# Performance work log

Hardware: AMD Instinct MI355X
Metric: run time of the kernel (lower is better)

Reference implementation:

```python
import jax, jax.numpy as jnp
import numpy as np

B, C, N = 8, 512, 2048  # batch, channels (=size), tokens


def setup_inputs() -> dict:
    key = jax.random.key(0)
    ks = jax.random.split(key, 9)
    s = 1.0 / np.sqrt(C)
    return {
        "q": jax.random.normal(ks[0], (B, C, N), dtype=jnp.float32),
        "k": jax.random.normal(ks[1], (B, C, N), dtype=jnp.float32),
        "v": jax.random.normal(ks[2], (B, C, N), dtype=jnp.float32),
        "wq": jax.random.normal(ks[3], (C, C), dtype=jnp.float32) * s,
        "bq": jax.random.normal(ks[4], (C,), dtype=jnp.float32) * s,
        "wk": jax.random.normal(ks[5], (C, C), dtype=jnp.float32) * s,
        "bk": jax.random.normal(ks[6], (C,), dtype=jnp.float32) * s,
        "wv": jax.random.normal(ks[7], (C, C), dtype=jnp.float32) * s,
        "bv": jax.random.normal(ks[8], (C,), dtype=jnp.float32) * s,
    }


def _proj(x, w, b):
    # 1x1 conv over channels: out[b,c,n] = sum_i w[c,i] x[b,i,n] + b[c]
    return jnp.einsum('ci,bin->bcn', w, x) + b[None, :, None]


def reference(q, k, v, wq, bq, wk, bk, wv, bv):
    residual = q                                   # [B, C, N]
    qp = _proj(q, wq, bq).transpose(0, 2, 1)       # [B, N, C]
    kp = _proj(k, wk, bk).transpose(0, 2, 1)       # [B, N, C]
    vp = _proj(v, wv, bv).transpose(0, 2, 1)       # [B, N, C]
    attn = jnp.einsum('bnc,bmc->bnm', qp, kp)      # raw QK^T, no scale/softmax
    out = jnp.einsum('bnm,bmc->bnc', attn, vp)     # [B, N, C]
    return out.transpose(0, 2, 1) + residual       # [B, C, N]
```

## Files before the change

kernel.cpp:

```cpp
#include <hip/hip_runtime.h>
#include <hip/hip_bf16.h>
#include <stdint.h>

#define B_ 8
#define C_ 512
#define N_ 2048

typedef __bf16 bf16_t;
typedef bf16_t bf16x8 __attribute__((ext_vector_type(8)));
typedef bf16_t bf16x4 __attribute__((ext_vector_type(4)));
typedef float f32x4 __attribute__((ext_vector_type(4)));

__global__ __launch_bounds__(256) void prep_qw_kernel(
    const float* __restrict__ q,
    const float* __restrict__ wq, const float* __restrict__ wk,
    const float* __restrict__ wv, const float* __restrict__ bq,
    const float* __restrict__ bk,
    bf16_t* __restrict__ qT,
    bf16_t* __restrict__ WqT, bf16_t* __restrict__ WkT, bf16_t* __restrict__ Wvb,
    float* __restrict__ s1p)
{
    __shared__ bf16_t tile[64][65];
    __shared__ float red256[256];
    const int bid = blockIdx.x;
    const int tid = threadIdx.x;

    if (bid < 2048) {
        const int b = bid >> 8;
        const int rem = bid & 255;
        const int c0 = (rem >> 5) * 64;
        const int n0 = (rem & 31) * 64;
        const float* src = q + (size_t)b * C_ * N_;
        bf16_t* dT = qT + (size_t)b * N_ * C_;
        const int cx = (tid & 15) * 4, ry = tid >> 4;
#pragma unroll
        for (int r = ry; r < 64; r += 16) {
            float4 f = *(const float4*)&src[(size_t)(c0 + r) * N_ + n0 + cx];
            tile[r][cx + 0] = (bf16_t)f.x; tile[r][cx + 1] = (bf16_t)f.y;
            tile[r][cx + 2] = (bf16_t)f.z; tile[r][cx + 3] = (bf16_t)f.w;
        }
        __syncthreads();
#pragma unroll
        for (int r = ry; r < 64; r += 16) {
            bf16x4 o;
            o[0] = tile[cx + 0][r]; o[1] = tile[cx + 1][r];
            o[2] = tile[cx + 2][r]; o[3] = tile[cx + 3][r];
            *(bf16x4*)&dT[(size_t)(n0 + r) * C_ + c0 + cx] = o;
        }
    } else if (bid < 2176) {
        const int t = bid - 2048;
        const float* src = (t < 64) ? wq : wk;
        bf16_t* dst = (t < 64) ? WqT : WkT;
        const int j = t & 63;
        const int i0 = (j & 7) * 64, c0 = (j >> 3) * 64;
        const int cx = (tid & 15) * 4, ry = tid >> 4;
#pragma unroll
        for (int r = ry; r < 64; r += 16) {
            float4 f = *(const float4*)&src[(size_t)(c0 + r) * C_ + i0 + cx];
            tile[r][cx + 0] = (bf16_t)f.x; tile[r][cx + 1] = (bf16_t)f.y;
            tile[r][cx + 2] = (bf16_t)f.z; tile[r][cx + 3] = (bf16_t)f.w;
        }
        __syncthreads();
#pragma unroll
        for (int r = ry; r < 64; r += 16) {
            bf16x4 o;
            o[0] = tile[cx + 0][r]; o[1] = tile[cx + 1][r];
            o[2] = tile[cx + 2][r]; o[3] = tile[cx + 3][r];
            *(bf16x4*)&dst[(size_t)(i0 + r) * C_ + c0 + cx] = o;
        }
    } else if (bid < 2240) {
        const int j = bid - 2176;
#pragma unroll
        for (int p = 0; p < 4; ++p) {
            const int i = j * 4096 + p * 1024 + tid * 4;
            float4 f = *(const float4*)(wv + i);
            bf16x4 o;
            o[0] = (bf16_t)f.x; o[1] = (bf16_t)f.y;
            o[2] = (bf16_t)f.z; o[3] = (bf16_t)f.w;
            *(bf16x4*)(Wvb + i) = o;
        }
    } else {
        float p = bk[tid] * bq[tid] + bk[tid + 256] * bq[tid + 256];
        red256[tid] = p;
        __syncthreads();
        for (int s = 128; s > 0; s >>= 1) {
            if (tid < s) red256[tid] += red256[tid + s];
            __syncthreads();
        }
        if (tid == 0) s1p[0] = red256[0];
    }
}

__global__ __launch_bounds__(256) void dkv_M_kernel(
    const float* __restrict__ Kin, const float* __restrict__ Vin,
    bf16_t* __restrict__ Dp, float* __restrict__ sk4, float* __restrict__ sv4,
    const bf16_t* __restrict__ WqT, const bf16_t* __restrict__ WkT,
    bf16_t* __restrict__ M, const float* __restrict__ bq,
    const float* __restrict__ bk, float* __restrict__ gk,
    float* __restrict__ va)
{
    __shared__ __align__(16) float AsF[128 * 64];
    __shared__ __align__(16) float BsF[128 * 64];

    const int f = blockIdx.x;
    const int tid = threadIdx.x, lane = tid & 63, wave = tid >> 6;
    const int wr = wave >> 1, wc = wave & 1;
    const size_t sCC = (size_t)C_ * C_;

    if (f < 512) {
        const int xcd = f & 7, sl = f >> 3;
        const int g = xcd + 8 * (sl >> 4), t5 = sl & 15;
        const int bz = g >> 2, sp = g & 3;
        const int m0 = (t5 >> 2) * 128, n0 = (t5 & 3) * 128;
        const int kbeg = sp * 512;

        const float* Ab = Kin + (size_t)bz * C_ * N_;
        const float* Bb = Vin + (size_t)bz * C_ * N_;

        f32x4 acc[4][4];
#pragma unroll
        for (int i = 0; i < 4; ++i)
#pragma unroll
            for (int j = 0; j < 4; ++j) acc[i][j] = 0.f;

        const int prow = tid >> 4;
        const int cs   = (tid & 15) ^ (prow & 7);
        const int ldso = tid * 16;

        const int srr = tid >> 1, hh = tid & 1;
        float hsA = 0.f, hsB = 0.f;
        const bool doA = (n0 == 0), doB = (m0 == 0);

        for (int t = 0; t < 8; ++t) {
            const float* ga = Ab + (size_t)(m0 + prow) * N_ + kbeg + t * 64 + cs * 4;
            const float* gb = Bb + (size_t)(n0 + prow) * N_ + kbeg + t * 64 + cs * 4;
#pragma unroll
            for (int p = 0; p < 8; ++p)
                __builtin_amdgcn_global_load_lds(
                    (const __attribute__((address_space(1))) void*)(ga + (size_t)p * 16 * N_),
                    (__attribute__((address_space(3))) void*)((char*)AsF + ldso + p * 4096),
                    16, 0, 0);
#pragma unroll
            for (int p = 0; p < 8; ++p)
                __builtin_amdgcn_global_load_lds(
                    (const __attribute__((address_space(1))) void*)(gb + (size_t)p * 16 * N_),
                    (__attribute__((address_space(3))) void*)((char*)BsF + ldso + p * 4096),
                    16, 0, 0);
            __syncthreads();

#pragma unroll
            for (int kk = 0; kk < 64; kk += 32) {
                bf16x8 af[4], bfr[4];
                const int kcol = kk + (lane >> 4) * 8;
                const int c1 = kcol >> 2;
#pragma unroll
                for (int m = 0; m < 4; ++m) {
                    const int r = wr * 64 + (lane & 15) + m * 16;
                    f32x4 lo = *(const f32x4*)((const char*)AsF + r * 256 + ((c1 ^ (r & 7)) << 4));
                    f32x4 hi = *(const f32x4*)((const char*)AsF + r * 256 + (((c1 + 1) ^ (r & 7)) << 4));
                    bf16x8 fr;
                    fr[0] = (bf16_t)lo[0]; fr[1] = (bf16_t)lo[1];
                    fr[2] = (bf16_t)lo[2]; fr[3] = (bf16_t)lo[3];
                    fr[4] = (bf16_t)hi[0]; fr[5] = (bf16_t)hi[1];
                    fr[6] = (bf16_t)hi[2]; fr[7] = (bf16_t)hi[3];
                    af[m] = fr;
                }
#pragma unroll
                for (int n = 0; n < 4; ++n) {
                    const int r = wc * 64 + (lane & 15) + n * 16;
                    f32x4 lo = *(const f32x4*)((const char*)BsF + r * 256 + ((c1 ^ (r & 7)) << 4));
                    f32x4 hi = *(const f32x4*)((const char*)BsF + r * 256 + (((c1 + 1) ^ (r & 7)) << 4));
                    bf16x8 fr;
                    fr[0] = (bf16_t)lo[0]; fr[1] = (bf16_t)lo[1];
                    fr[2] = (bf16_t)lo[2]; fr[3] = (bf16_t)lo[3];
                    fr[4] = (bf16_t)hi[0]; fr[5] = (bf16_t)hi[1];
                    fr[6] = (bf16_t)hi[2]; fr[7] = (bf16_t)hi[3];
                    bfr[n] = fr;
                }
#pragma unroll
                for (int m = 0; m < 4; ++m)
#pragma unroll
                    for (int n = 0; n < 4; ++n)
                        acc[m][n] = __builtin_amdgcn_mfma_f32_16x16x32_bf16(
                            af[m], bfr[n], acc[m][n], 0, 0, 0);
            }

            if (doA) {
#pragma unroll
                for (int u = 0; u < 8; ++u) {
                    const int slot = ((hh * 8 + u) + srr) & 15;
                    f32x4 vv = *(const f32x4*)((const char*)AsF + srr * 256 + slot * 16);
                    hsA += vv[0] + vv[1] + vv[2] + vv[3];
                }
            }
            if (doB) {
#pragma unroll
                for (int u = 0; u < 8; ++u) {
                    const int slot = ((hh * 8 + u) + srr) & 15;
                    f32x4 vv = *(const f32x4*)((const char*)BsF + srr * 256 + slot * 16);
                    hsB += vv[0] + vv[1] + vv[2] + vv[3];
                }
            }
            __syncthreads();
        }

        const int rj = (lane >> 4) * 4;
        const int cc = lane & 15;
        const int z = bz * 4 + sp;
#pragma unroll
        for (int m = 0; m < 4; ++m)
#pragma unroll
            for (int n = 0; n < 4; ++n) {
                const int col = n0 + wc * 64 + n * 16 + cc;
                f32x4 vv = acc[m][n];
#pragma unroll
                for (int j = 0; j < 4; ++j) {
                    const int row = m0 + wr * 64 + m * 16 + rj + j;
                    Dp[(size_t)z * sCC + (size_t)row * C_ + col] = (bf16_t)vv[j];
                }
            }
        if (doA) {
            hsA += __shfl_xor(hsA, 1, 64);
            if (!hh) sk4[(size_t)(sp * B_ + bz) * C_ + m0 + srr] = hsA;
        }
        if (doB) {
            hsB += __shfl_xor(hsB, 1, 64);
            if (!hh) sv4[(size_t)(sp * B_ + bz) * C_ + n0 + srr] = hsB;
        }
    } else if (f < 576) {
        bf16_t* As = (bf16_t*)AsF;
        bf16_t* Bs = (bf16_t*)BsF;
        const int g = f - 512;
        const int m0 = (g >> 3) * 64, n0 = (g & 7) * 64;
        f32x4 acc[2][2];
#pragma unroll
        for (int i = 0; i < 2; ++i)
#pragma unroll
            for (int j = 0; j < 2; ++j) acc[i][j] = 0.f;
        const int srow = tid >> 3;
        const int scol = ((tid & 7) ^ (srow & 7)) * 8;
        const int ldso = tid * 16;
        for (int t = 0; t < 8; ++t) {
            const bf16_t* ga = WqT + (size_t)(m0 + srow) * C_ + t * 64 + scol;
            const bf16_t* gb = WkT + (size_t)(n0 + srow) * C_ + t * 64 + scol;
#pragma unroll
            for (int p = 0; p < 2; ++p)
                __builtin_amdgcn_global_load_lds(
                    (const __attribute__((address_space(1))) void*)(ga + (size_t)p * 32 * C_),
                    (__attribute__((address_space(3))) void*)((char*)As + ldso + p * 4096),
                    16, 0, 0);
#pragma unroll
            for (int p = 0; p < 2; ++p)
                __builtin_amdgcn_global_load_lds(
                    (const __attribute__((address_space(1))) void*)(gb + (size_t)p * 32 * C_),
                    (__attribute__((address_space(3))) void*)((char*)Bs + ldso + p * 4096),
                    16, 0, 0);
            __syncthreads();
#pragma unroll
            for (int kk = 0; kk < 64; kk += 32) {
                bf16x8 af[2], bfr[2];
                const int kcol = kk + (lane >> 4) * 8;
                const int kcn = kcol >> 3;
#pragma unroll
                for (int m = 0; m < 2; ++m) {
                    const int r = wr * 32 + (lane & 15) + m * 16;
                    af[m] = *(const bf16x8*)((const char*)As + r * 128 +
                                             ((kcn ^ (r & 7)) << 4));
                }
#pragma unroll
                for (int n = 0; n < 2; ++n) {
                    const int r = wc * 32 + (lane & 15) + n * 16;
                    bfr[n] = *(const bf16x8*)((const char*)Bs + r * 128 +
                                              ((kcn ^ (r & 7)) << 4));
                }
#pragma unroll
                for (int m = 0; m < 2; ++m)
#pragma unroll
                    for (int n = 0; n < 2; ++n)
                        acc[m][n] = __builtin_amdgcn_mfma_f32_16x16x32_bf16(
                            af[m], bfr[n], acc[m][n], 0, 0, 0);
            }
            __syncthreads();
        }
        const int rj = (lane >> 4) * 4;
        const int cc = lane & 15;
#pragma unroll
        for (int m = 0; m < 2; ++m)
#pragma unroll
            for (int n = 0; n < 2; ++n) {
                const int col = n0 + wc * 32 + n * 16 + cc;
                f32x4 vv = acc[m][n];
#pragma unroll
                for (int j = 0; j < 4; ++j) {
                    const int row = m0 + wr * 32 + m * 16 + rj + j;
                    M[(size_t)row * C_ + col] = (bf16_t)vv[j];
                }
            }
    } else {
        const int j = f - 576;
        const bf16_t* W = (j < 8) ? WkT : WqT;
        const float* bb = (j < 8) ? bq : bk;
        float* out = (j < 8) ? gk : va;
        const int row = (j & 7) * 64 + (tid >> 2);
        const int c0 = (tid & 3) * 128;
        const bf16_t* rp = W + (size_t)row * C_ + c0;
        float acc = 0.f;
#pragma unroll
        for (int e = 0; e < 128; e += 8) {
            bf16x8 vv = *(const bf16x8*)(rp + e);
#pragma unroll
            for (int x = 0; x < 8; ++x) acc += (float)vv[x] * bb[c0 + e + x];
        }
        acc += __shfl_xor(acc, 1, 64);
        acc += __shfl_xor(acc, 2, 64);
        if ((tid & 3) == 0) out[row] = acc;
    }
}

__global__ __launch_bounds__(256) void p1_fused_kernel(
    const bf16_t* __restrict__ Wvb, const bf16_t* __restrict__ Dp,
    bf16_t* __restrict__ P1, const bf16_t* __restrict__ M,
    const float* __restrict__ sk4, const float* __restrict__ sv4,
    const float* __restrict__ gk, const float* __restrict__ s1p,
    float* __restrict__ u, float* __restrict__ vbraw, float* __restrict__ s2)
{
    __shared__ __align__(16) bf16_t As[64 * 64];
    __shared__ __align__(16) bf16_t Bs[64 * 64];
    __shared__ float svec[C_];
    __shared__ float red[256];
    const int f = blockIdx.x;
    const int tid = threadIdx.x, lane = tid & 63, wave = tid >> 6;
    const int wr = wave >> 1, wc = wave & 1;
    const size_t sCC = (size_t)C_ * C_;
    const size_t st = (size_t)B_ * C_;

    if (f < 512) {
        const int bz = f >> 6;
        const int m0 = ((f >> 3) & 7) * 64, n0 = (f & 7) * 64;
        f32x4 acc[2][2];
#pragma unroll
        for (int i = 0; i < 2; ++i)
#pragma unroll
            for (int j = 0; j < 2; ++j) acc[i][j] = 0.f;
        const int srow = tid >> 3;
        const int scol = ((tid & 7) ^ (srow & 7)) * 8;
        const int ldso = tid * 16;

        for (int sp = 0; sp < 4; ++sp) {
            const bf16_t* Bb = Dp + (size_t)(bz * 4 + sp) * sCC;
            for (int t = 0; t < 8; ++t) {
                const bf16_t* ga = Wvb + (size_t)(m0 + srow) * C_ + t * 64 + scol;
                const bf16_t* gb = Bb + (size_t)(n0 + srow) * C_ + t * 64 + scol;
#pragma unroll
                for (int p = 0; p < 2; ++p)
                    __builtin_amdgcn_global_load_lds(
                        (const __attribute__((address_space(1))) void*)(ga + (size_t)p * 32 * C_),
                        (__attribute__((address_space(3))) void*)((char*)As + ldso + p * 4096),
                        16, 0, 0);
#pragma unroll
                for (int p = 0; p < 2; ++p)
                    __builtin_amdgcn_global_load_lds(
                        (const __attribute__((address_space(1))) void*)(gb + (size_t)p * 32 * C_),
                        (__attribute__((address_space(3))) void*)((char*)Bs + ldso + p * 4096),
                        16, 0, 0);
                __syncthreads();
#pragma unroll
                for (int kk = 0; kk < 64; kk += 32) {
                    bf16x8 af[2], bfr[2];
                    const int kcol = kk + (lane >> 4) * 8;
                    const int kcn = kcol >> 3;
#pragma unroll
                    for (int m = 0; m < 2; ++m) {
                        const int r = wr * 32 + (lane & 15) + m * 16;
                        af[m] = *(const bf16x8*)((const char*)As + r * 128 +
                                                 ((kcn ^ (r & 7)) << 4));
                    }
#pragma unroll
                    for (int n = 0; n < 2; ++n) {
                        const int r = wc * 32 + (lane & 15) + n * 16;
                        bfr[n] = *(const bf16x8*)((const char*)Bs + r * 128 +
                                                  ((kcn ^ (r & 7)) << 4));
                    }
#pragma unroll
                    for (int m = 0; m < 2; ++m)
#pragma unroll
                        for (int n = 0; n < 2; ++n)
                            acc[m][n] = __builtin_amdgcn_mfma_f32_16x16x32_bf16(
                                af[m], bfr[n], acc[m][n], 0, 0, 0);
                }
                __syncthreads();
            }
        }
        const int rj = (lane >> 4) * 4;
        const int cc = lane & 15;
#pragma unroll
        for (int m = 0; m < 2; ++m)
#pragma unroll
            for (int n = 0; n < 2; ++n) {
                const int col = n0 + wc * 32 + n * 16 + cc;
                f32x4 vv = acc[m][n];
#pragma unroll
                for (int j = 0; j < 4; ++j) {
                    const int row = m0 + wr * 32 + m * 16 + rj + j;
                    P1[(size_t)bz * sCC + (size_t)row * C_ + col] = (bf16_t)vv[j];
                }
            }
    } else if (f < 520) {
        const int b = f - 512;
        const float* s4 = sv4 + (size_t)b * C_;
#pragma unroll
        for (int rr = 0; rr < 2; ++rr) {
            const int j = tid * 2 + rr;
            svec[j] = s4[j] + s4[st + j] + s4[2 * st + j] + s4[3 * st + j];
        }
        __syncthreads();
        const int c = tid * 2;
#pragma unroll
        for (int rr = 0; rr < 2; ++rr) {
            const bf16_t* row = Wvb + (size_t)(c + rr) * C_;
            float acc = 0.f;
            for (int j = 0; j < C_; j += 8) {
                bf16x8 vv = *(const bf16x8*)(row + j);
#pragma unroll
                for (int e = 0; e < 8; ++e) acc += (float)vv[e] * svec[j + e];
            }
            u[b * C_ + c + rr] = acc;
        }
    } else {
        const int b = f - 520;
        const float* s4 = sk4 + (size_t)b * C_;
#pragma unroll
        for (int rr = 0; rr < 2; ++rr) {
            const int j = tid * 2 + rr;
            svec[j] = s4[j] + s4[st + j] + s4[2 * st + j] + s4[3 * st + j];
        }
        __syncthreads();
        const int c = tid * 2;
#pragma unroll
        for (int rr = 0; rr < 2; ++rr) {
            const bf16_t* row = M + (size_t)(c + rr) * C_;
            float acc = 0.f;
            for (int j = 0; j < C_; j += 8) {
                bf16x8 vv = *(const bf16x8*)(row + j);
#pragma unroll
                for (int e = 0; e < 8; ++e) acc += (float)vv[e] * svec[j + e];
            }
            vbraw[b * C_ + c + rr] = acc;
        }
        float p = svec[tid] * gk[tid] + svec[tid + 256] * gk[tid + 256];
        red[tid] = p;
        __syncthreads();
        for (int s = 128; s > 0; s >>= 1) {
            if (tid < s) red[tid] += red[tid + s];
            __syncthreads();
        }
        if (tid == 0) s2[b] = red[0] + 2048.0f * s1p[0];
    }
}

__global__ __launch_bounds__(256) void gemm_ht(
    const bf16_t* __restrict__ A, const bf16_t* __restrict__ Bm,
    bf16_t* __restrict__ Cout,
    const float* __restrict__ e0, const float* __restrict__ e1,
    const float* __restrict__ e2, const float* __restrict__ e3,
    const float* __restrict__ bqv, float* __restrict__ hout,
    const float* __restrict__ s1p, const float* __restrict__ s2p)
{
    __shared__ __align__(16) bf16_t As[64 * 64];
    __shared__ __align__(16) bf16_t Bs[64 * 64];

    const int tid = threadIdx.x, lane = tid & 63, wave = tid >> 6;
    const int wr = wave >> 1, wc = wave & 1;
    const int bz = blockIdx.z;
    const int m0 = blockIdx.y * 64, n0 = blockIdx.x * 64;
    const size_t sCC = (size_t)C_ * C_;

    const bf16_t* Ab = A + (size_t)bz * sCC;

    f32x4 acc[2][2];
#pragma unroll
    for (int i = 0; i < 2; ++i)
#pragma unroll
        for (int j = 0; j < 2; ++j) acc[i][j] = 0.f;

    const int srow = tid >> 3;
    const int scol = ((tid & 7) ^ (srow & 7)) * 8;
    const int ldso = tid * 16;

    float hacc = 0.f;
    const bool doH = (blockIdx.x == 0);

    for (int t = 0; t < 8; ++t) {
        const bf16_t* ga = Ab + (size_t)(m0 + srow) * C_ + t * 64 + scol;
        const bf16_t* gb = Bm + (size_t)(n0 + srow) * C_ + t * 64 + scol;
#pragma unroll
        for (int p = 0; p < 2; ++p)
            __builtin_amdgcn_global_load_lds(
                (const __attribute__((address_space(1))) void*)(ga + (size_t)p * 32 * C_),
                (__attribute__((address_space(3))) void*)((char*)As + ldso + p * 4096),
                16, 0, 0);
#pragma unroll
        for (int p = 0; p < 2; ++p)
            __builtin_amdgcn_global_load_lds(
                (const __attribute__((address_space(1))) void*)(gb + (size_t)p * 32 * C_),
                (__attribute__((address_space(3))) void*)((char*)Bs + ldso + p * 4096),
                16, 0, 0);
        __syncthreads();

#pragma unroll
        for (int kk = 0; kk < 64; kk += 32) {
            bf16x8 af[2], bfr[2];
            const int kcol = kk + (lane >> 4) * 8;
            const int kcn = kcol >> 3;
#pragma unroll
            for (int m = 0; m < 2; ++m) {
                const int r = wr * 32 + (lane & 15) + m * 16;
                af[m] = *(const bf16x8*)((const char*)As + r * 128 +
                                         ((kcn ^ (r & 7)) << 4));
            }
#pragma unroll
            for (int n = 0; n < 2; ++n) {
                const int r = wc * 32 + (lane & 15) + n * 16;
                bfr[n] = *(const bf16x8*)((const char*)Bs + r * 128 +
                                          ((kcn ^ (r & 7)) << 4));
            }
#pragma unroll
            for (int m = 0; m < 2; ++m)
#pragma unroll
                for (int n = 0; n < 2; ++n)
                    acc[m][n] = __builtin_amdgcn_mfma_f32_16x16x32_bf16(
                        af[m], bfr[n], acc[m][n], 0, 0, 0);
        }
        if (doH) {
            const int rr = tid >> 2, qq = tid & 3;
#pragma unroll
            for (int uq = 0; uq < 2; ++uq) {
                const int c = qq * 2 + uq;
                bf16x8 av = *(const bf16x8*)((const char*)As + rr * 128 +
                                             ((c ^ (rr & 7)) << 4));
                const float* bp = bqv + t * 64 + c * 8;
#pragma unroll
                for (int e = 0; e < 8; ++e) hacc += (float)av[e] * bp[e];
            }
        }
        __syncthreads();
    }

    const int rj = (lane >> 4) * 4;
    const int cc = lane & 15;
#pragma unroll
    for (int m = 0; m < 2; ++m) {
#pragma unroll
        for (int n = 0; n < 2; ++n) {
            const int col = n0 + wc * 32 + n * 16 + cc;
            f32x4 vv = acc[m][n];
#pragma unroll
            for (int j = 0; j < 4; ++j) {
                const int row = m0 + wr * 32 + m * 16 + rj + j;
                float val = vv[j] + e0[bz * C_ + row] * e1[col] +
                            e2[row] * (e3[bz * C_ + col] + 2048.0f * e1[col]);
                Cout[(size_t)bz * sCC + (size_t)row * C_ + col] = (bf16_t)val;
            }
        }
    }
    if (doH) {
        hacc += __shfl_xor(hacc, 1, 64);
        hacc += __shfl_xor(hacc, 2, 64);
        if ((tid & 3) == 0) {
            const int row = m0 + (tid >> 2);
            hout[bz * C_ + row] = hacc + e0[bz * C_ + row] * s1p[0] +
                                  e2[row] * s2p[bz];
        }
    }
}

__global__ __launch_bounds__(256) void gemm_final(
    const bf16_t* __restrict__ A, const bf16_t* __restrict__ Bm,
    float* __restrict__ Cout, const float* __restrict__ qres,
    const float* __restrict__ hvec)
{
    __shared__ __align__(16) bf16_t As[128 * 64];
    __shared__ __align__(16) bf16_t Bs[128 * 64];

    const int f = blockIdx.x;
    const int xcd = f & 7, sl = f >> 3;
    const int g = xcd + 8 * (sl >> 2);
    const int m0 = (sl & 3) * 128;
    const int bz = g >> 4;
    const int n0 = (g & 15) * 128;
    const int K = C_;

    const int tid = threadIdx.x, lane = tid & 63, wave = tid >> 6;
    const int wr = wave >> 1, wc = wave & 1;

    const bf16_t* Ab = A + (size_t)bz * ((size_t)C_ * C_);
    const bf16_t* Bb = Bm + (size_t)bz * ((size_t)N_ * C_);

    f32x4 acc[4][4];
#pragma unroll
    for (int i = 0; i < 4; ++i)
#pragma unroll
        for (int j = 0; j < 4; ++j) acc[i][j] = 0.f;

    const int srow = tid >> 3;
    const int scol = ((tid & 7) ^ (srow & 7)) * 8;
    const int ldso = tid * 16;

    for (int t = 0; t < 8; ++t) {
        const bf16_t* ga = Ab + (size_t)(m0 + srow) * K + t * 64 + scol;
        const bf16_t* gb = Bb + (size_t)(n0 + srow) * K + t * 64 + scol;
#pragma unroll
        for (int p = 0; p < 4; ++p)
            __builtin_amdgcn_global_load_lds(
                (const __attribute__((address_space(1))) void*)(ga + (size_t)p * 32 * K),
                (__attribute__((address_space(3))) void*)((char*)As + ldso + p * 4096),
                16, 0, 0);
#pragma unroll
        for (int p = 0; p < 4; ++p)
            __builtin_amdgcn_global_load_lds(
                (const __attribute__((address_space(1))) void*)(gb + (size_t)p * 32 * K),
                (__attribute__((address_space(3))) void*)((char*)Bs + ldso + p * 4096),
                16, 0, 0);
        __syncthreads();

#pragma unroll
        for (int kk = 0; kk < 64; kk += 32) {
            bf16x8 af[4], bfr[4];
            const int kcol = kk + (lane >> 4) * 8;
            const int kcn = kcol >> 3;
#pragma unroll
            for (int m = 0; m < 4; ++m) {
                const int r = wr * 64 + (lane & 15) + m * 16;
                af[m] = *(const bf16x8*)((const char*)As + r * 128 +
                                         ((kcn ^ (r & 7)) << 4));
            }
#pragma unroll
            for (int n = 0; n < 4; ++n) {
                const int r = wc * 64 + (lane & 15) + n * 16;
                bfr[n] = *(const bf16x8*)((const char*)Bs + r * 128 +
                                          ((kcn ^ (r & 7)) << 4));
            }
#pragma unroll
            for (int m = 0; m < 4; ++m)
#pragma unroll
                for (int n = 0; n < 4; ++n)
                    acc[m][n] = __builtin_amdgcn_mfma_f32_16x16x32_bf16(
                        af[m], bfr[n], acc[m][n], 0, 0, 0);
        }
        __syncthreads();
    }

    const int rj = (lane >> 4) * 4;
    const int cc = lane & 15;
    const size_t ob = (size_t)bz * ((size_t)C_ * N_);
#pragma unroll
    for (int m = 0; m < 4; ++m) {
#pragma unroll
        for (int n = 0; n < 4; ++n) {
            const int col = n0 + wc * 64 + n * 16 + cc;
            f32x4 vv = acc[m][n];
#pragma unroll
            for (int j = 0; j < 4; ++j) {
                const int row = m0 + wr * 64 + m * 16 + rj + j;
                const size_t o = ob + (size_t)row * N_ + col;
                Cout[o] = vv[j] + hvec[bz * C_ + row] + qres[o];
            }
        }
    }
}

extern "C" void kernel_launch(void* const* d_in, const int* in_sizes, int n_in,
                              void* d_out, int out_size, void* d_ws, size_t ws_size,
                              hipStream_t stream)
{
    (void)in_sizes; (void)n_in; (void)out_size; (void)ws_size;
    const float* q  = (const float*)d_in[0];
    const float* k  = (const float*)d_in[1];
    const float* v  = (const float*)d_in[2];
    const float* wq = (const float*)d_in[3];
    const float* bq = (const float*)d_in[4];
    const float* wk = (const float*)d_in[5];
    const float* bk = (const float*)d_in[6];
    const float* wv = (const float*)d_in[7];
    const float* bv = (const float*)d_in[8];
    float* out = (float*)d_out;

    char* ws = (char*)d_ws;
    const size_t WSZ = (size_t)C_ * C_ * 2;
    const size_t TSZ = (size_t)B_ * N_ * C_ * 2;
    const size_t SCZ = (size_t)B_ * C_ * C_ * 2;
    const size_t VSZ = (size_t)B_ * C_ * 4;
    size_t off = 0;
    bf16_t* WqTb = (bf16_t*)(ws + off); off += WSZ;
    bf16_t* WkTb = (bf16_t*)(ws + off); off += WSZ;
    bf16_t* Wvb  = (bf16_t*)(ws + off); off += WSZ;
    bf16_t* M    = (bf16_t*)(ws + off); off += WSZ;
    bf16_t* qT   = (bf16_t*)(ws + off); off += TSZ;
    bf16_t* Dp   = (bf16_t*)(ws + off); off += TSZ;
    bf16_t* P1   = (bf16_t*)(ws + off); off += SCZ;
    bf16_t* HT   = (bf16_t*)(ws + off); off += SCZ;
    float*  sk4  = (float*)(ws + off);  off += 4 * VSZ;
    float*  sv4  = (float*)(ws + off);  off += 4 * VSZ;
    float*  gk   = (float*)(ws + off);  off += C_ * 4;
    float*  va   = (float*)(ws + off);  off += C_ * 4;
    float*  s1p  = (float*)(ws + off);  off += 64;
    float*  s2   = (float*)(ws + off);  off += 64;
    float*  uu   = (float*)(ws + off);  off += VSZ;
    float*  vbr  = (float*)(ws + off);  off += VSZ;
    float*  hb   = (float*)(ws + off);  off += VSZ;

    const dim3 blk(256);

    prep_qw_kernel<<<dim3(2241), blk, 0, stream>>>(
        q, wq, wk, wv, bq, bk, qT, WqTb, WkTb, Wvb, s1p);

    dkv_M_kernel<<<dim3(592), blk, 0, stream>>>(
        k, v, Dp, sk4, sv4, WqTb, WkTb, M, bq, bk, gk, va);

    p1_fused_kernel<<<dim3(528), blk, 0, stream>>>(
        Wvb, Dp, P1, M, sk4, sv4, gk, s1p, uu, vbr, s2);

    gemm_ht<<<dim3(8, 8, B_), blk, 0, stream>>>(
        P1, M, HT, uu, va, bv, vbr, gk, hb, s1p, s2);

    gemm_final<<<dim3(512), blk, 0, stream>>>(HT, qT, out, q, hb);
}
```

Measured before the change: 102.7 us.

## Merge prep and K/V covariance kernels into one launch, move M build later

Fuses the q/weight transpose-and-cast prep kernel with the K·Vᵀ partial GEMM into a single mega kernel. Block indices interleave GEMM tiles with transpose tiles so both kinds of work share the GPU, and one kernel boundary is removed. The M = WqᵀWk GEMM and the gk/va reductions move into the P1 kernel. The vbraw computation is rewritten to go through Wk (fp32) and then WqT instead of reading M, because M is no longer ready at that point. The cost is a more complex dispatch inside the kernel and extra matrix-vector work per batch.

```diff
diff --git a/kernel.cpp b/kernel.cpp
--- a/kernel.cpp
+++ b/kernel.cpp
@@ -11,94 +11,17 @@
 typedef bf16_t bf16x4 __attribute__((ext_vector_type(4)));
 typedef float f32x4 __attribute__((ext_vector_type(4)));
 
-__global__ __launch_bounds__(256) void prep_qw_kernel(
+__global__ __launch_bounds__(256) void mega_kernel(
+    const float* __restrict__ Kin, const float* __restrict__ Vin,
     const float* __restrict__ q,
     const float* __restrict__ wq, const float* __restrict__ wk,
     const float* __restrict__ wv, const float* __restrict__ bq,
     const float* __restrict__ bk,
+    bf16_t* __restrict__ Dp, float* __restrict__ sk4, float* __restrict__ sv4,
     bf16_t* __restrict__ qT,
     bf16_t* __restrict__ WqT, bf16_t* __restrict__ WkT, bf16_t* __restrict__ Wvb,
     float* __restrict__ s1p)
 {
-    __shared__ bf16_t tile[64][65];
-    __shared__ float red256[256];
-    const int bid = blockIdx.x;
-    const int tid = threadIdx.x;
-
-    if (bid < 2048) {
-        const int b = bid >> 8;
-        const int rem = bid & 255;
-        const int c0 = (rem >> 5) * 64;
-        const int n0 = (rem & 31) * 64;
-        const float* src = q + (size_t)b * C_ * N_;
-        bf16_t* dT = qT + (size_t)b * N_ * C_;
-        const int cx = (tid & 15) * 4, ry = tid >> 4;
-#pragma unroll
-        for (int r = ry; r < 64; r += 16) {
-            float4 f = *(const float4*)&src[(size_t)(c0 + r) * N_ + n0 + cx];
-            tile[r][cx + 0] = (bf16_t)f.x; tile[r][cx + 1] = (bf16_t)f.y;
-            tile[r][cx + 2] = (bf16_t)f.z; tile[r][cx + 3] = (bf16_t)f.w;
-        }
-        __syncthreads();
-#pragma unroll
-        for (int r = ry; r < 64; r += 16) {
-            bf16x4 o;
-            o[0] = tile[cx + 0][r]; o[1] = tile[cx + 1][r];
-            o[2] = tile[cx + 2][r]; o[3] = tile[cx + 3][r];
-            *(bf16x4*)&dT[(size_t)(n0 + r) * C_ + c0 + cx] = o;
-        }
-    } else if (bid < 2176) {
-        const int t = bid - 2048;
-        const float* src = (t < 64) ? wq : wk;
-        bf16_t* dst = (t < 64) ? WqT : WkT;
-        const int j = t & 63;
-        const int i0 = (j & 7) * 64, c0 = (j >> 3) * 64;
-        const int cx = (tid & 15) * 4, ry = tid >> 4;
-#pragma unroll
-        for (int r = ry; r < 64; r += 16) {
-            float4 f = *(const float4*)&src[(size_t)(c0 + r) * C_ + i0 + cx];
-            tile[r][cx + 0] = (bf16_t)f.x; tile[r][cx + 1] = (bf16_t)f.y;
-            tile[r][cx + 2] = (bf16_t)f.z; tile[r][cx + 3] = (bf16_t)f.w;
-        }
-        __syncthreads();
-#pragma unroll
-        for (int r = ry; r < 64; r += 16) {
-            bf16x4 o;
-            o[0] = tile[cx + 0][r]; o[1] = tile[cx + 1][r];
-            o[2] = tile[cx + 2][r]; o[3] = tile[cx + 3][r];
-            *(bf16x4*)&dst[(size_t)(i0 + r) * C_ + c0 + cx] = o;
-        }
-    } else if (bid < 2240) {
-        const int j = bid - 2176;
-#pragma unroll
-        for (int p = 0; p < 4; ++p) {
-            const int i = j * 4096 + p * 1024 + tid * 4;
-            float4 f = *(const float4*)(wv + i);
-            bf16x4 o;
-            o[0] = (bf16_t)f.x; o[1] = (bf16_t)f.y;
-            o[2] = (bf16_t)f.z; o[3] = (bf16_t)f.w;
-            *(bf16x4*)(Wvb + i) = o;
-        }
-    } else {
-        float p = bk[tid] * bq[tid] + bk[tid + 256] * bq[tid + 256];
-        red256[tid] = p;
-        __syncthreads();
-        for (int s = 128; s > 0; s >>= 1) {
-            if (tid < s) red256[tid] += red256[tid + s];
-            __syncthreads();
-        }
-        if (tid == 0) s1p[0] = red256[0];
-    }
-}
-
-__global__ __launch_bounds__(256) void dkv_M_kernel(
-    const float* __restrict__ Kin, const float* __restrict__ Vin,
-    bf16_t* __restrict__ Dp, float* __restrict__ sk4, float* __restrict__ sv4,
-    const bf16_t* __restrict__ WqT, const bf16_t* __restrict__ WkT,
-    bf16_t* __restrict__ M, const float* __restrict__ bq,
-    const float* __restrict__ bk, float* __restrict__ gk,
-    float* __restrict__ va)
-{
     __shared__ __align__(16) float AsF[128 * 64];
     __shared__ __align__(16) float BsF[128 * 64];
 
@@ -107,10 +30,23 @@
     const int wr = wave >> 1, wc = wave & 1;
     const size_t sCC = (size_t)C_ * C_;
 
-    if (f < 512) {
-        const int xcd = f & 7, sl = f >> 3;
-        const int g = xcd + 8 * (sl >> 4), t5 = sl & 15;
-        const int bz = g >> 2, sp = g & 3;
+    int gemm_id = -1, tr_id = -1, w_id = -1;
+    if (f < 1024) {
+        const int hi = f >> 4, lo = f & 15;
+        if (lo < 8) gemm_id = hi * 8 + lo;
+        else        tr_id = hi * 8 + (lo - 8);
+    } else if (f < 2560) {
+        tr_id = (f - 1024) + 512;
+    } else if (f < 2752) {
+        w_id = f - 2560;
+    }
+
+    if (gemm_id >= 0) {
+        const int g = gemm_id;
+        const int xcd = g & 7;
+        const int grp = xcd * 4 + (g >> 7);
+        const int t5 = (g >> 3) & 15;
+        const int bz = grp >> 2, sp = grp & 3;
         const int m0 = (t5 >> 2) * 128, n0 = (t5 & 3) * 128;
         const int kbeg = sp * 512;
 
@@ -227,9 +163,172 @@
             hsB += __shfl_xor(hsB, 1, 64);
             if (!hh) sv4[(size_t)(sp * B_ + bz) * C_ + n0 + srr] = hsB;
         }
+    } else if (tr_id >= 0) {
+        bf16_t (*tile)[65] = (bf16_t(*)[65])AsF;
+        const int t = tr_id;
+        const int b = t >> 8;
+        const int rem = t & 255;
+        const int c0 = (rem >> 5) * 64;
+        const int n0 = (rem & 31) * 64;
+        const float* src = q + (size_t)b * C_ * N_;
+        bf16_t* dT = qT + (size_t)b * N_ * C_;
+        const int cx = (tid & 15) * 4, ry = tid >> 4;
+#pragma unroll
+        for (int r = ry; r < 64; r += 16) {
+            float4 ff = *(const float4*)&src[(size_t)(c0 + r) * N_ + n0 + cx];
+            tile[r][cx + 0] = (bf16_t)ff.x; tile[r][cx + 1] = (bf16_t)ff.y;
+            tile[r][cx + 2] = (bf16_t)ff.z; tile[r][cx + 3] = (bf16_t)ff.w;
+        }
+        __syncthreads();
+#pragma unroll
+        for (int r = ry; r < 64; r += 16) {
+            bf16x4 o;
+            o[0] = tile[cx + 0][r]; o[1] = tile[cx + 1][r];
+            o[2] = tile[cx + 2][r]; o[3] = tile[cx + 3][r];
+            *(bf16x4*)&dT[(size_t)(n0 + r) * C_ + c0 + cx] = o;
+        }
+    } else if (w_id >= 0) {
+        const int t = w_id;
+        if (t < 128) {
+            bf16_t (*tile)[65] = (bf16_t(*)[65])AsF;
+            const float* src = (t < 64) ? wq : wk;
+            bf16_t* dst = (t < 64) ? WqT : WkT;
+            const int j = t & 63;
+            const int i0 = (j & 7) * 64, c0 = (j >> 3) * 64;
+            const int cx = (tid & 15) * 4, ry = tid >> 4;
+#pragma unroll
+            for (int r = ry; r < 64; r += 16) {
+                float4 ff = *(const float4*)&src[(size_t)(c0 + r) * C_ + i0 + cx];
+                tile[r][cx + 0] = (bf16_t)ff.x; tile[r][cx + 1] = (bf16_t)ff.y;
+                tile[r][cx + 2] = (bf16_t)ff.z; tile[r][cx + 3] = (bf16_t)ff.w;
+            }
+            __syncthreads();
+#pragma unroll
+            for (int r = ry; r < 64; r += 16) {
+                bf16x4 o;
+                o[0] = tile[cx + 0][r]; o[1] = tile[cx + 1][r];
+                o[2] = tile[cx + 2][r]; o[3] = tile[cx + 3][r];
+                *(bf16x4*)&dst[(size_t)(i0 + r) * C_ + c0 + cx] = o;
+            }
+        } else {
+            const int j = t - 128;
+#pragma unroll
+            for (int p = 0; p < 4; ++p) {
+                const int i = j * 4096 + p * 1024 + tid * 4;
+                float4 ff = *(const float4*)(wv + i);
+                bf16x4 o;
+                o[0] = (bf16_t)ff.x; o[1] = (bf16_t)ff.y;
+                o[2] = (bf16_t)ff.z; o[3] = (bf16_t)ff.w;
+                *(bf16x4*)(Wvb + i) = o;
+            }
+        }
+    } else {
+        float* red = AsF;
+        float p = bk[tid] * bq[tid] + bk[tid + 256] * bq[tid + 256];
+        red[tid] = p;
+        __syncthreads();
+        for (int s = 128; s > 0; s >>= 1) {
+            if (tid < s) red[tid] += red[tid + s];
+            __syncthreads();
+        }
+        if (tid == 0) s1p[0] = red[0];
+    }
+}
+
+__global__ __launch_bounds__(256) void p1_fused_kernel(
+    const bf16_t* __restrict__ Wvb, const bf16_t* __restrict__ Dp,
+    bf16_t* __restrict__ P1,
+    const bf16_t* __restrict__ WqT, const bf16_t* __restrict__ WkT,
+    bf16_t* __restrict__ M, const float* __restrict__ wkf,
+    const float* __restrict__ bq, const float* __restrict__ bk,
+    const float* __restrict__ sk4, const float* __restrict__ sv4,
+    const float* __restrict__ s1p,
+    float* __restrict__ gk, float* __restrict__ va,
+    float* __restrict__ u, float* __restrict__ vbraw, float* __restrict__ s2)
+{
+    __shared__ __align__(16) bf16_t As[64 * 64];
+    __shared__ __align__(16) bf16_t Bs[64 * 64];
+    __shared__ float svec[C_];
+    __shared__ float tv[C_];
+    __shared__ float red[256];
+    const int f = blockIdx.x;
+    const int tid = threadIdx.x, lane = tid & 63, wave = tid >> 6;
+    const int wr = wave >> 1, wc = wave & 1;
+    const size_t sCC = (size_t)C_ * C_;
+    const size_t st = (size_t)B_ * C_;
+
+    if (f < 512) {
+        const int bz = f >> 6;
+        const int m0 = ((f >> 3) & 7) * 64, n0 = (f & 7) * 64;
+        f32x4 acc[2][2];
+#pragma unroll
+        for (int i = 0; i < 2; ++i)
+#pragma unroll
+            for (int j = 0; j < 2; ++j) acc[i][j] = 0.f;
+        const int srow = tid >> 3;
+        const int scol = ((tid & 7) ^ (srow & 7)) * 8;
+        const int ldso = tid * 16;
+
+        for (int sp = 0; sp < 4; ++sp) {
+            const bf16_t* Bb = Dp + (size_t)(bz * 4 + sp) * sCC;
+            for (int t = 0; t < 8; ++t) {
+                const bf16_t* ga = Wvb + (size_t)(m0 + srow) * C_ + t * 64 + scol;
+                const bf16_t* gb = Bb + (size_t)(n0 + srow) * C_ + t * 64 + scol;
+#pragma unroll
+                for (int p = 0; p < 2; ++p)
+                    __builtin_amdgcn_global_load_lds(
+                        (const __attribute__((address_space(1))) void*)(ga + (size_t)p * 32 * C_),
+                        (__attribute__((address_space(3))) void*)((char*)As + ldso + p * 4096),
+                        16, 0, 0);
+#pragma unroll
+                for (int p = 0; p < 2; ++p)
+                    __builtin_amdgcn_global_load_lds(
+                        (const __attribute__((address_space(1))) void*)(gb + (size_t)p * 32 * C_),
+                        (__attribute__((address_space(3))) void*)((char*)Bs + ldso + p * 4096),
+                        16, 0, 0);
+                __syncthreads();
+#pragma unroll
+                for (int kk = 0; kk < 64; kk += 32) {
+                    bf16x8 af[2], bfr[2];
+                    const int kcol = kk + (lane >> 4) * 8;
+                    const int kcn = kcol >> 3;
+#pragma unroll
+                    for (int m = 0; m < 2; ++m) {
+                        const int r = wr * 32 + (lane & 15) + m * 16;
+                        af[m] = *(const bf16x8*)((const char*)As + r * 128 +
+                                                 ((kcn ^ (r & 7)) << 4));
+                    }
+#pragma unroll
+                    for (int n = 0; n < 2; ++n) {
+                        const int r = wc * 32 + (lane & 15) + n * 16;
+                        bfr[n] = *(const bf16x8*)((const char*)Bs + r * 128 +
+                                                  ((kcn ^ (r & 7)) << 4));
+                    }
+#pragma unroll
+                    for (int m = 0; m < 2; ++m)
+#pragma unroll
+                        for (int n = 0; n < 2; ++n)
+                            acc[m][n] = __builtin_amdgcn_mfma_f32_16x16x32_bf16(
+                                af[m], bfr[n], acc[m][n], 0, 0, 0);
+                }
+                __syncthreads();
+            }
+        }
+        const int rj = (lane >> 4) * 4;
+        const int cc = lane & 15;
+#pragma unroll
+        for (int m = 0; m < 2; ++m)
+#pragma unroll
+            for (int n = 0; n < 2; ++n) {
+                const int col = n0 + wc * 32 + n * 16 + cc;
+                f32x4 vv = acc[m][n];
+#pragma unroll
+                for (int j = 0; j < 4; ++j) {
+                    const int row = m0 + wr * 32 + m * 16 + rj + j;
+                    P1[(size_t)bz * sCC + (size_t)row * C_ + col] = (bf16_t)vv[j];
+                }
+            }
     } else if (f < 576) {
-        bf16_t* As = (bf16_t*)AsF;
-        bf16_t* Bs = (bf16_t*)BsF;
         const int g = f - 512;
         const int m0 = (g >> 3) * 64, n0 = (g & 7) * 64;
         f32x4 acc[2][2];
@@ -296,7 +395,7 @@
                     M[(size_t)row * C_ + col] = (bf16_t)vv[j];
                 }
             }
-    } else {
+    } else if (f < 592) {
         const int j = f - 576;
         const bf16_t* W = (j < 8) ? WkT : WqT;
         const float* bb = (j < 8) ? bq : bk;
@@ -314,99 +413,8 @@
         acc += __shfl_xor(acc, 1, 64);
         acc += __shfl_xor(acc, 2, 64);
         if ((tid & 3) == 0) out[row] = acc;
-    }
-}
-
-__global__ __launch_bounds__(256) void p1_fused_kernel(
-    const bf16_t* __restrict__ Wvb, const bf16_t* __restrict__ Dp,
-    bf16_t* __restrict__ P1, const bf16_t* __restrict__ M,
-    const float* __restrict__ sk4, const float* __restrict__ sv4,
-    const float* __restrict__ gk, const float* __restrict__ s1p,
-    float* __restrict__ u, float* __restrict__ vbraw, float* __restrict__ s2)
-{
-    __shared__ __align__(16) bf16_t As[64 * 64];
-    __shared__ __align__(16) bf16_t Bs[64 * 64];
-    __shared__ float svec[C_];
-    __shared__ float red[256];
-    const int f = blockIdx.x;
-    const int tid = threadIdx.x, lane = tid & 63, wave = tid >> 6;
-    const int wr = wave >> 1, wc = wave & 1;
-    const size_t sCC = (size_t)C_ * C_;
-    const size_t st = (size_t)B_ * C_;
-
-    if (f < 512) {
-        const int bz = f >> 6;
-        const int m0 = ((f >> 3) & 7) * 64, n0 = (f & 7) * 64;
-        f32x4 acc[2][2];
-#pragma unroll
-        for (int i = 0; i < 2; ++i)
-#pragma unroll
-            for (int j = 0; j < 2; ++j) acc[i][j] = 0.f;
-        const int srow = tid >> 3;
-        const int scol = ((tid & 7) ^ (srow & 7)) * 8;
-        const int ldso = tid * 16;
-
-        for (int sp = 0; sp < 4; ++sp) {
-            const bf16_t* Bb = Dp + (size_t)(bz * 4 + sp) * sCC;
-            for (int t = 0; t < 8; ++t) {
-                const bf16_t* ga = Wvb + (size_t)(m0 + srow) * C_ + t * 64 + scol;
-                const bf16_t* gb = Bb + (size_t)(n0 + srow) * C_ + t * 64 + scol;
-#pragma unroll
-                for (int p = 0; p < 2; ++p)
-                    __builtin_amdgcn_global_load_lds(
-                        (const __attribute__((address_space(1))) void*)(ga + (size_t)p * 32 * C_),
-                        (__attribute__((address_space(3))) void*)((char*)As + ldso + p * 4096),
-                        16, 0, 0);
-#pragma unroll
-                for (int p = 0; p < 2; ++p)
-                    __builtin_amdgcn_global_load_lds(
-                        (const __attribute__((address_space(1))) void*)(gb + (size_t)p * 32 * C_),
-                        (__attribute__((address_space(3))) void*)((char*)Bs + ldso + p * 4096),
-                        16, 0, 0);
-                __syncthreads();
-#pragma unroll
-                for (int kk = 0; kk < 64; kk += 32) {
-                    bf16x8 af[2], bfr[2];
-                    const int kcol = kk + (lane >> 4) * 8;
-                    const int kcn = kcol >> 3;
-#pragma unroll
-                    for (int m = 0; m < 2; ++m) {
-                        const int r = wr * 32 + (lane & 15) + m * 16;
-                        af[m] = *(const bf16x8*)((const char*)As + r * 128 +
-                                                 ((kcn ^ (r & 7)) << 4));
-                    }
-#pragma unroll
-                    for (int n = 0; n < 2; ++n) {
-                        const int r = wc * 32 + (lane & 15) + n * 16;
-                        bfr[n] = *(const bf16x8*)((const char*)Bs + r * 128 +
-                                                  ((kcn ^ (r & 7)) << 4));
-                    }
-#pragma unroll
-                    for (int m = 0; m < 2; ++m)
-#pragma unroll
-                        for (int n = 0; n < 2; ++n)
-                            acc[m][n] = __builtin_amdgcn_mfma_f32_16x16x32_bf16(
-                                af[m], bfr[n], acc[m][n], 0, 0, 0);
-                }
-                __syncthreads();
-            }
-        }
-        const int rj = (lane >> 4) * 4;
-        const int cc = lane & 15;
-#pragma unroll
-        for (int m = 0; m < 2; ++m)
-#pragma unroll
-            for (int n = 0; n < 2; ++n) {
-                const int col = n0 + wc * 32 + n * 16 + cc;
-                f32x4 vv = acc[m][n];
-#pragma unroll
-                for (int j = 0; j < 4; ++j) {
-                    const int row = m0 + wr * 32 + m * 16 + rj + j;
-                    P1[(size_t)bz * sCC + (size_t)row * C_ + col] = (bf16_t)vv[j];
-                }
-            }
-    } else if (f < 520) {
-        const int b = f - 512;
+    } else if (f < 600) {
+        const int b = f - 592;
         const float* s4 = sv4 + (size_t)b * C_;
 #pragma unroll
         for (int rr = 0; rr < 2; ++rr) {
@@ -427,7 +435,7 @@
             u[b * C_ + c + rr] = acc;
         }
     } else {
-        const int b = f - 520;
+        const int b = f - 600;
         const float* s4 = sk4 + (size_t)b * C_;
 #pragma unroll
         for (int rr = 0; rr < 2; ++rr) {
@@ -438,16 +446,28 @@
         const int c = tid * 2;
 #pragma unroll
         for (int rr = 0; rr < 2; ++rr) {
-            const bf16_t* row = M + (size_t)(c + rr) * C_;
+            const float* row = wkf + (size_t)(c + rr) * C_;
+            float acc = 0.f;
+            for (int j = 0; j < C_; j += 4) {
+                float4 ww = *(const float4*)(row + j);
+                acc += ww.x * svec[j] + ww.y * svec[j + 1] +
+                       ww.z * svec[j + 2] + ww.w * svec[j + 3];
+            }
+            tv[c + rr] = acc;
+        }
+        __syncthreads();
+#pragma unroll
+        for (int rr = 0; rr < 2; ++rr) {
+            const bf16_t* row = WqT + (size_t)(c + rr) * C_;
             float acc = 0.f;
             for (int j = 0; j < C_; j += 8) {
                 bf16x8 vv = *(const bf16x8*)(row + j);
 #pragma unroll
-                for (int e = 0; e < 8; ++e) acc += (float)vv[e] * svec[j + e];
+                for (int e = 0; e < 8; ++e) acc += (float)vv[e] * tv[j + e];
             }
             vbraw[b * C_ + c + rr] = acc;
         }
-        float p = svec[tid] * gk[tid] + svec[tid + 256] * gk[tid + 256];
+        float p = bq[tid] * tv[tid] + bq[tid + 256] * tv[tid + 256];
         red[tid] = p;
         __syncthreads();
         for (int s = 128; s > 0; s >>= 1) {
@@ -711,14 +731,12 @@
 
     const dim3 blk(256);
 
-    prep_qw_kernel<<<dim3(2241), blk, 0, stream>>>(
-        q, wq, wk, wv, bq, bk, qT, WqTb, WkTb, Wvb, s1p);
-
-    dkv_M_kernel<<<dim3(592), blk, 0, stream>>>(
-        k, v, Dp, sk4, sv4, WqTb, WkTb, M, bq, bk, gk, va);
-
-    p1_fused_kernel<<<dim3(528), blk, 0, stream>>>(
-        Wvb, Dp, P1, M, sk4, sv4, gk, s1p, uu, vbr, s2);
+    mega_kernel<<<dim3(2753), blk, 0, stream>>>(
+        k, v, q, wq, wk, wv, bq, bk, Dp, sk4, sv4, qT, WqTb, WkTb, Wvb, s1p);
+
+    p1_fused_kernel<<<dim3(608), blk, 0, stream>>>(
+        Wvb, Dp, P1, WqTb, WkTb, M, wk, bq, bk, sk4, sv4, s1p,
+        gk, va, uu, vbr, s2);
 
     gemm_ht<<<dim3(8, 8, B_), blk, 0, stream>>>(
         P1, M, HT, uu, va, bv, vbr, gk, hb, s1p, s2);
```

New measurement: 142.4 us. 38.7% more time.
